# Kernel optimization log

Measured on AMD Instinct MI355X. Metric: run time of the kernel, lower is better.

Reference implementation:

```python
import jax, jax.numpy as jnp
import numpy as np

B_, L_, D_ = 2, 4096, 1024
E_ = 2
DI = E_ * D_            # 2048
H_ = 16
HD_ = DI // H_          # 128
N_ = 128
K_ = 4                  # d_conv
CS_ = 256               # SSD chunk size
MC_ = 256               # Hebbian memory chunk size
ALPHA = 0.5             # memory_alpha (== write_alpha default)


def _silu(x):
    return x * jax.nn.sigmoid(x)


def _rmsnorm(x, w, eps=1e-6):
    return x * jax.lax.rsqrt(jnp.mean(x * x, axis=-1, keepdims=True) + eps) * w


def setup_inputs() -> dict:
    key = jax.random.key(0)
    ks = jax.random.split(key, 8)
    proj_dim = 2 * DI + 2 * H_ * N_ + H_
    n = lambda k, sh, sc: jax.random.normal(k, sh, jnp.float32) * sc
    return {
        "x": n(ks[0], (B_, L_, D_), 1.0),
        "norm_w": jnp.ones((D_,), jnp.float32),
        "w_in": n(ks[1], (proj_dim, D_), 0.02),
        "conv_w": n(ks[2], (DI, K_), 0.2),
        "conv_b": jnp.zeros((DI,), jnp.float32),
        "A_log": jnp.log(2.0 * jnp.ones((H_,), jnp.float32)),
        "dt_bias": jnp.zeros((H_,), jnp.float32),
        "D_skip": jnp.ones((DI,), jnp.float32),
        "w_out": n(ks[3], (D_, DI), 0.02),
        "w_write": n(ks[4], (D_, D_), 0.02),
        "w_read": n(ks[5], (D_, D_), 0.02),
        "decay": jnp.float32(4.6),
    }


def _forward(x, norm_w, w_in, conv_w, conv_b, A_log, dt_bias, D_skip,
             w_out, w_write, w_read, decay):
    B, L, D = x.shape
    residual = x
    xn = _rmsnorm(x, norm_w)

    # ---- SSDBlock ----
    proj = xn @ w_in.T  # (B,L,2*DI+2*H*N+H)
    val = proj[..., :DI]
    gate = proj[..., DI:2 * DI]
    Bp = proj[..., 2 * DI:2 * DI + H_ * N_].reshape(B, L, H_, N_)
    Cp = proj[..., 2 * DI + H_ * N_:2 * DI + 2 * H_ * N_].reshape(B, L, H_, N_)
    dt = jax.nn.softplus(proj[..., -H_:] + dt_bias)  # (B,L,H)

    # causal depthwise conv1d (kernel K_, groups=DI)
    vp = jnp.pad(val, ((0, 0), (K_ - 1, 0), (0, 0)))
    val = sum(conv_w[:, k] * vp[:, k:k + L, :] for k in range(K_)) + conv_b
    val = _silu(val).reshape(B, L, H_, HD_)

    ld = dt * (-jnp.exp(A_log))  # log decay (B,L,H)

    nc = L // CS_
    to_chunks = lambda a: jnp.moveaxis(a.reshape(B, nc, CS_, *a.shape[2:]), 1, 0)
    tril = jnp.tril(jnp.ones((CS_, CS_), bool))
    Dv = D_skip.reshape(1, H_, 1, HD_)

    def ssd_chunk(h, inp):
        v_c, b_c, c_c, ld_c = inp  # (B,CS,H,HD), (B,CS,H,N), (B,CS,H,N), (B,CS,H)
        cum = jnp.cumsum(ld_c, axis=1)            # (B,CS,H)
        cum_h = jnp.transpose(cum, (0, 2, 1))     # (B,H,CS)
        dd = cum_h[:, :, :, None] - cum_h[:, :, None, :]
        Lmat = jnp.where(tril, jnp.exp(dd), 0.0)
        M = jnp.einsum('blhn,bmhn->bhlm', c_c, b_c) * Lmat
        v_h = jnp.transpose(v_c, (0, 2, 1, 3))    # (B,H,CS,HD)
        Y = M @ v_h
        Y = Y + jnp.einsum('blhn,bhdn,blh->bhld', c_c, h, jnp.exp(cum))
        Y = Y + Dv * v_h
        h = jnp.exp(cum[:, -1])[:, :, None, None] * h + \
            jnp.einsum('blhd,blhn,blh->bhdn', v_c, b_c, jnp.exp(cum[:, -1:, :] - cum))
        return h, Y

    h0 = jnp.zeros((B, H_, HD_, N_), jnp.float32)
    _, Ys = jax.lax.scan(ssd_chunk, h0,
                         (to_chunks(val), to_chunks(Bp), to_chunks(Cp), to_chunks(ld)))
    # (nc,B,H,CS,HD) -> (B,L,DI)
    Y = jnp.transpose(Ys, (1, 0, 3, 2, 4)).reshape(B, L, DI)
    out = (Y * _silu(gate)) @ w_out.T  # (B,L,D)

    # ---- Hebbian memory (chunkwise) ----
    gamma = jax.nn.sigmoid(decay)
    lg = jnp.log(gamma)
    v = out @ w_write.T
    wk = jnp.pad(out[:, :-1], ((0, 0), (1, 0), (0, 0)))  # shifted write keys
    p = jnp.arange(MC_)
    diffs = jnp.maximum(p[:, None] - 1 - p[None, :], 0).astype(jnp.float32)
    causal = (p[:, None] > p[None, :]).astype(jnp.float32)
    Mmem = jnp.exp(diffs * lg) * causal
    gp = gamma ** p                    # read decay by position in chunk
    gw = gamma ** (MC_ - 1 - p)        # write decay to end of chunk
    nm = L // MC_
    tom = lambda a: jnp.moveaxis(a.reshape(B, nm, MC_, D), 1, 0)

    def mem_chunk(W, inp):
        rk_c, wk_c, v_c = inp  # (B,MC,D)
        inter = jnp.einsum('bde,bte->btd', W, rk_c) * gp[None, :, None]
        S = jnp.einsum('bie,bje->bij', rk_c, wk_c)
        intra = (S * Mmem) @ v_c
        W = gamma ** MC_ * W + jnp.einsum('btd,bte->bde', v_c * gw[None, :, None], wk_c)
        return W, inter + intra

    W0 = jnp.zeros((B, D, D), jnp.float32)
    _, reads = jax.lax.scan(mem_chunk, W0, (tom(out), tom(wk), tom(v)))
    reads = jnp.moveaxis(reads, 0, 1).reshape(B, L, D)
    out = out + ALPHA * (reads @ w_read.T)
    return residual + out


def reference(x, norm_w, w_in, conv_w, conv_b, A_log, dt_bias, D_skip,
              w_out, w_write, w_read, decay):
    return _forward(x, norm_w, w_in, conv_w, conv_b, A_log, dt_bias, D_skip,
                    w_out, w_write, w_read, decay)
```

## Files before the change

kernel.cpp:

```cpp
#include <hip/hip_runtime.h>
#include <hip/hip_bf16.h>

typedef __hip_bfloat16 bf16;
typedef __attribute__((ext_vector_type(8))) short short8;
typedef __attribute__((ext_vector_type(4))) float floatx4;
typedef __attribute__((ext_vector_type(16))) float floatx16;

#define B_ 2
#define L_ 4096
#define D_ 1024
#define DI_ 2048
#define H_ 16
#define HD_ 128
#define N_ 128
#define CS_ 256
#define MC_ 256
#define NC_ 16
#define PROJ_ 8208

__device__ __forceinline__ float bf2f(short s) {
    return __uint_as_float(((unsigned)(unsigned short)s) << 16);
}

__device__ __forceinline__ void gl_lds16(const void* g, void* s) {
    __builtin_amdgcn_global_load_lds(
        (const __attribute__((address_space(1))) void*)g,
        (__attribute__((address_space(3))) void*)s, 16, 0, 0);
}

struct GemmP {
    const bf16* A; const bf16* Bt;
    float* C; bf16* CB; bf16* CB2; bf16* CB3;
    const float* add0; const float* add1; const bf16* add0b; const float* scr;
    long lda, ldb, ldc;
    int M, N, K, zinner;
    long a_zo, a_zi, b_zo, b_zi, c_zo, c_zi;
};

template<int EPI>
__global__ __launch_bounds__(256, 2) void gemm_bt(GemmP p)
{
    int NT = gridDim.x, MT = gridDim.y;
    long T = (long)NT * MT * gridDim.z;
    long flat = ((long)blockIdx.z * MT + blockIdx.y) * NT + blockIdx.x;
    int xcd = (int)(flat & 7);
    long q = flat >> 3;
    long Tq = T >> 3; int Tr = (int)(T & 7);
    long tile = (long)xcd * Tq + (long)(xcd < Tr ? xcd : Tr) + q;
    long per_z = (long)NT * MT;
    int z = (int)(tile / per_z);
    int t2 = (int)(tile - (long)z * per_z);
    int FG = NT >> 3;
    int g, width, within;
    if (t2 < FG * MT * 8) { g = t2 / (MT * 8); width = 8; within = t2 - g * MT * 8; }
    else                  { g = FG; width = NT - FG * 8; within = t2 - FG * MT * 8; }
    int m_outer = within / (8 * width);
    int hb = MT - m_outer * 8; if (hb > 8) hb = 8;
    int inner = within - m_outer * 8 * width;
    int n_in = inner / hb, m_in = inner - n_in * hb;
    int m0 = (m_outer * 8 + m_in) * 128;
    int n0 = (g * 8 + n_in) * 128;

    int zo = z / p.zinner, zi = z % p.zinner;
    const bf16* A  = p.A  + (long)zo * p.a_zo + (long)zi * p.a_zi;
    const bf16* Bt = p.Bt + (long)zo * p.b_zo + (long)zi * p.b_zi;
    long coff = (long)zo * p.c_zo + (long)zi * p.c_zi;

    __shared__ __align__(16) bf16 As[128 * 64];
    __shared__ __align__(16) bf16 Bs[128 * 64];

    int tid = threadIdx.x;
    int lane = tid & 63, wave = tid >> 6;
    int wm = (wave >> 1) * 64, wn = (wave & 1) * 64;
    int ln31 = lane & 31, hi = lane >> 5;

    floatx16 acc[2][2];
#pragma unroll
    for (int i = 0; i < 2; i++)
#pragma unroll
        for (int j = 0; j < 2; j++)
#pragma unroll
            for (int r = 0; r < 16; r++) acc[i][j][r] = 0.f;

    int lrow = lane >> 3;
    int lc = ((lane & 7) ^ lrow) * 8;
    int wrow = wave * 32;
    int rx = lane & 7;

    for (int k0 = 0; k0 < p.K; k0 += 64) {
#pragma unroll
        for (int t = 0; t < 4; t++) {
            int row = wrow + t * 8 + lrow;
            gl_lds16(A + (long)(m0 + row) * p.lda + k0 + lc, &As[(wrow + t * 8) * 64]);
            int bn = n0 + row; if (bn > p.N - 1) bn = p.N - 1;
            gl_lds16(Bt + (long)bn * p.ldb + k0 + lc, &Bs[(wrow + t * 8) * 64]);
        }
        __syncthreads();
#pragma unroll
        for (int ks = 0; ks < 64; ks += 16) {
            int lb = (ks >> 3) + hi;
            int po = ((lb ^ rx) << 3);
            short8 af[2], bq[2];
#pragma unroll
            for (int i = 0; i < 2; i++)
                af[i] = *(const short8*)&As[(wm + i * 32 + ln31) * 64 + po];
#pragma unroll
            for (int j = 0; j < 2; j++)
                bq[j] = *(const short8*)&Bs[(wn + j * 32 + ln31) * 64 + po];
#pragma unroll
            for (int i = 0; i < 2; i++)
#pragma unroll
                for (int j = 0; j < 2; j++)
                    acc[i][j] = __builtin_amdgcn_mfma_f32_32x32x16_bf16(af[i], bq[j], acc[i][j], 0, 0, 0);
        }
        __syncthreads();
    }

#pragma unroll
    for (int i = 0; i < 2; i++) {
#pragma unroll
        for (int j = 0; j < 2; j++) {
#pragma unroll
            for (int r = 0; r < 16; r++) {
                int gm = m0 + wm + i * 32 + (r & 3) + 8 * (r >> 2) + 4 * hi;
                int gn = n0 + wn + j * 32 + ln31;
                if (gm >= p.M || gn >= p.N) continue;
                float a = acc[i][j][r];
                if (EPI == 0) {
                    p.C[coff + (long)gm * p.ldc + gn] = a;
                } else if (EPI == 2) {
                    if (gn < 2048)      p.CB [(long)gm * 2048 + gn]          = __float2bfloat16(a);
                    else if (gn < 4096) p.CB2[(long)gm * 2048 + (gn - 2048)] = __float2bfloat16(a);
                    else if (gn < 8192) p.CB3[(long)gm * 4096 + (gn - 4096)] = __float2bfloat16(a);
                    else                p.C  [(long)gm * 16   + (gn - 8192)] = a;
                } else if (EPI == 3) {
                    float lg = p.scr[1];
                    float v = (gm > gn) ? a * __expf((float)(gm - 1 - gn) * lg) : 0.f;
                    p.CB[coff + (long)gm * p.ldc + gn] = __float2bfloat16(v);
                } else if (EPI == 4) {
                    long ix = coff + (long)gm * p.ldc + gn;
                    float t = a * p.scr[16 + gm] + __bfloat162float(p.add0b[ix]);
                    p.CB[ix] = __float2bfloat16(t);
                } else if (EPI == 6) {
                    p.CB[coff + (long)gm * p.ldc + gn] = __float2bfloat16(a);
                } else if (EPI == 7) {
                    long ix = (long)gm * p.ldc + gn;
                    p.C[ix] = p.add0[ix] + __bfloat162float(p.add0b[ix]) + 0.5f * a;
                } else if (EPI == 8) {
                    long ix = (long)gm * p.ldc + gn;
                    bf16 v = __float2bfloat16(a);
                    p.CB[ix] = v;
                    int l = gm & (L_ - 1);
                    if (l != L_ - 1) p.CB2[ix + p.ldc] = v;
                    if (l == 0) p.CB2[ix] = __float2bfloat16(0.f);
                }
            }
        }
    }
}

__global__ void k_gamma(const float* decay, float* scr)
{
    int t = threadIdx.x;
    float g = 1.f / (1.f + expf(-decay[0]));
    float lg = logf(g);
    if (t == 0) { scr[0] = g; scr[1] = lg; scr[2] = expf(256.f * lg); }
    scr[16 + t]  = expf(lg * (float)t);
    scr[272 + t] = expf(lg * (float)(255 - t));
}

__global__ void k_f2ball(const float* __restrict__ s0, bf16* __restrict__ d0, long n0,
                         const float* __restrict__ s1, bf16* __restrict__ d1, long n1,
                         const float* __restrict__ s2, bf16* __restrict__ d2, long n2,
                         const float* __restrict__ s3, bf16* __restrict__ d3, long n3)
{
    long i = (long)blockIdx.x * 256 + threadIdx.x;
    const float* s; bf16* d; long rel = i;
    if (rel < n0) { s = s0; d = d0; }
    else { rel -= n0;
        if (rel < n1) { s = s1; d = d1; }
        else { rel -= n1;
            if (rel < n2) { s = s2; d = d2; }
            else { rel -= n2; if (rel >= n3) return; s = s3; d = d3; }
        }
    }
    float4 v = ((const float4*)s)[rel];
    bf16* o = d + rel * 4;
    o[0] = __float2bfloat16(v.x); o[1] = __float2bfloat16(v.y);
    o[2] = __float2bfloat16(v.z); o[3] = __float2bfloat16(v.w);
}

__global__ __launch_bounds__(256) void k_rmsnorm(const float* __restrict__ x,
                                                 const float* __restrict__ w,
                                                 bf16* __restrict__ o)
{
    int row = blockIdx.x, t = threadIdx.x;
    float4 xv = ((const float4*)(x + (long)row * D_))[t];
    float s = xv.x*xv.x + xv.y*xv.y + xv.z*xv.z + xv.w*xv.w;
#pragma unroll
    for (int m = 32; m > 0; m >>= 1) s += __shfl_xor(s, m, 64);
    __shared__ float ps[4];
    if ((t & 63) == 0) ps[t >> 6] = s;
    __syncthreads();
    s = ps[0] + ps[1] + ps[2] + ps[3];
    float r = rsqrtf(s * (1.f / (float)D_) + 1e-6f);
    float4 wv = ((const float4*)w)[t];
    bf16* orow = o + (long)row * D_ + t * 4;
    orow[0] = __float2bfloat16(xv.x * r * wv.x);
    orow[1] = __float2bfloat16(xv.y * r * wv.y);
    orow[2] = __float2bfloat16(xv.z * r * wv.z);
    orow[3] = __float2bfloat16(xv.w * r * wv.w);
}

__global__ __launch_bounds__(256) void k_cum(const float* __restrict__ dtr,
                                             const float* __restrict__ dt_bias,
                                             const float* __restrict__ A_log,
                                             float* __restrict__ cum_g,
                                             float* __restrict__ cumlast)
{
    int bid = blockIdx.x;
    int h = bid & 15, c = (bid >> 4) & 15, b = bid >> 8;
    long rowbase = (long)b * L_ + c * CS_;
    int tid = threadIdx.x;
    __shared__ float cum_s[256];
    float d = dtr[(rowbase + tid) * H_ + h] + dt_bias[h];
    float sp = (d > 20.f) ? d : log1pf(__expf(d));
    cum_s[tid] = -__expf(A_log[h]) * sp;
    __syncthreads();
    for (int off = 1; off < 256; off <<= 1) {
        float add = (tid >= off) ? cum_s[tid - off] : 0.f;
        __syncthreads();
        cum_s[tid] += add;
        __syncthreads();
    }
    cum_g[(rowbase + tid) * H_ + h] = cum_s[tid];
    if (tid == 255) cumlast[bid] = cum_s[255];
}

__global__ void k_vtc(const bf16* __restrict__ val_b, const float* __restrict__ cw,
                      const float* __restrict__ cb, bf16* __restrict__ vT)
{
    __shared__ bf16 tile[35][33];
    int b = blockIdx.z;
    int r0 = blockIdx.x * 32, c0 = blockIdx.y * 32;
    int tid = threadIdx.x;
    for (int idx = tid; idx < 35 * 32; idx += 256) {
        int row = idx >> 5, ch = idx & 31;
        int gl = r0 - 3 + row;
        bf16 v = __float2bfloat16(0.f);
        if (gl >= 0 && gl < L_) v = val_b[((long)b * L_ + gl) * 2048 + c0 + ch];
        tile[row][ch] = v;
    }
    __syncthreads();
    int tx = tid & 31, ty = tid >> 5;
    int l = r0 + tx;
    for (int i = 0; i < 32; i += 8) {
        int ch = c0 + ty + i;
        float4 cwv = ((const float4*)cw)[ch];
        float acc = cb[ch]
                  + cwv.x * __bfloat162float(tile[tx][ty + i])
                  + cwv.y * __bfloat162float(tile[tx + 1][ty + i])
                  + cwv.z * __bfloat162float(tile[tx + 2][ty + i])
                  + cwv.w * __bfloat162float(tile[tx + 3][ty + i]);
        float s = acc / (1.f + __expf(-acc));
        vT[((long)b * 2048 + ch) * L_ + l] = __float2bfloat16(s);
    }
}

__global__ void k_bt(const bf16* __restrict__ bc, bf16* __restrict__ BT)
{
    __shared__ bf16 tile[32][33];
    int b = blockIdx.z;
    int r0 = blockIdx.x * 32, c0 = blockIdx.y * 32;
    int tx = threadIdx.x & 31, ty = threadIdx.x >> 5;
    for (int i = 0; i < 32; i += 8)
        tile[ty + i][tx] = bc[((long)b * L_ + r0 + ty + i) * 4096 + c0 + tx];
    __syncthreads();
    int l = r0 + tx;
    for (int i = 0; i < 32; i += 8) {
        int col = c0 + ty + i;
        BT[((long)b * 2048 + col) * L_ + l] = tile[tx][ty + i];
    }
}

__global__ __launch_bounds__(256, 2) void k_ssd_u2(
    const bf16* __restrict__ vT, const bf16* __restrict__ BT,
    const float* __restrict__ cum_g, const float* __restrict__ cumlast,
    float* __restrict__ U)
{
    int bid = blockIdx.x;
    int h = bid & 15, c = (bid >> 4) & 15, b = bid >> 8;
    long rowbase = (long)b * L_ + c * CS_;
    int tid = threadIdx.x;
    __shared__ float w_s[256];
    w_s[tid] = __expf(cumlast[bid] - cum_g[(rowbase + tid) * H_ + h]);
    __syncthreads();
    int lane = tid & 63, wave = tid >> 6;
    int r16 = lane & 15, q8 = (lane >> 4) * 8, rq = (lane >> 4) * 4;
    int d0 = (wave >> 1) * 64, n0 = (wave & 1) * 64;
    const bf16* vb = vT + ((long)b * 2048 + h * 128) * L_ + c * 256;
    const bf16* bb = BT + ((long)b * 2048 + h * 128) * L_ + c * 256;
    floatx4 zero4 = {0.f, 0.f, 0.f, 0.f};
    floatx4 acc[4][4];
#pragma unroll
    for (int i = 0; i < 4; i++)
#pragma unroll
        for (int j = 0; j < 4; j++) acc[i][j] = zero4;
#pragma unroll 2
    for (int ks = 0; ks < 8; ks++) {
        float wv[8];
#pragma unroll
        for (int j = 0; j < 8; j++) wv[j] = w_s[ks * 32 + q8 + j];
        short8 af[4], bq[4];
#pragma unroll
        for (int i = 0; i < 4; i++) {
            short8 raw = *(const short8*)(vb + (long)(d0 + i * 16 + r16) * L_ + ks * 32 + q8);
#pragma unroll
            for (int j = 0; j < 8; j++) {
                float f = bf2f(raw[j]) * wv[j];
                raw[j] = (short)(__float_as_uint(f) >> 16);
            }
            af[i] = raw;
        }
#pragma unroll
        for (int j = 0; j < 4; j++)
            bq[j] = *(const short8*)(bb + (long)(n0 + j * 16 + r16) * L_ + ks * 32 + q8);
#pragma unroll
        for (int i = 0; i < 4; i++)
#pragma unroll
            for (int j = 0; j < 4; j++)
                acc[i][j] = __builtin_amdgcn_mfma_f32_16x16x32_bf16(af[i], bq[j], acc[i][j], 0, 0, 0);
    }
    float* up = U + (((long)c * B_ + b) * H_ + h) * 16384;
#pragma unroll
    for (int i = 0; i < 4; i++)
#pragma unroll
        for (int j = 0; j < 4; j++)
#pragma unroll
            for (int r = 0; r < 4; r++)
                up[(d0 + i * 16 + rq + r) * 128 + (n0 + j * 16 + r16)] = acc[i][j][r];
}

__global__ void k_ssd2(const float* __restrict__ U, const float* __restrict__ cumlast,
                       bf16* __restrict__ hst)
{
    long idx = (long)blockIdx.x * 256 + threadIdx.x;
    const long tot = (long)B_ * H_ * HD_ * N_;
    if (idx >= tot) return;
    int bh = (int)(idx >> 14);
    int b = bh >> 4, h = bh & 15;
    float hv = 0.f;
    for (int c = 0; c < NC_; c++) {
        hst[c * tot + idx] = __float2bfloat16(hv);
        float ef = __expf(cumlast[b * 256 + c * 16 + h]);
        hv = ef * hv + U[c * tot + idx];
    }
}

__global__ __launch_bounds__(256, 2) void k_ssd_y(
    const bf16* __restrict__ bc_b, const bf16* __restrict__ vT,
    const bf16* __restrict__ hst, const float* __restrict__ cum_g,
    const float* __restrict__ Dskip, const bf16* __restrict__ gate_b,
    bf16* __restrict__ yg)
{
    int bid = blockIdx.x;
    int h = bid & 15, c = (bid >> 4) & 15, b = bid >> 8;
    long rowbase = (long)b * L_ + c * CS_;
    int tid = threadIdx.x, lane = tid & 63, wave = tid >> 6;
    int r16 = lane & 15, q8 = (lane >> 4) * 8, rq = (lane >> 4) * 4;
    int wt = (wave >> 1) * 32, wmS = (wave & 1) * 32, wd = (wave & 1) * 64;

    __shared__ float cum_s[256];
    __shared__ __align__(16) bf16 Ss[64][72];

    cum_s[tid] = cum_g[(rowbase + tid) * H_ + h];
    __syncthreads();

    const bf16* Cb  = bc_b + rowbase * 4096 + 2048 + h * 128;
    const bf16* Bb  = bc_b + rowbase * 4096 + h * 128;
    const bf16* vTb = vT + ((long)b * 2048 + h * 128) * L_ + c * 256;
    const bf16* hp  = hst + (((long)c * B_ + b) * H_ + h) * 16384;

    floatx4 zero4 = {0.f, 0.f, 0.f, 0.f};

    for (int tt = 0; tt < 4; tt++) {
        int tbase = tt * 64;
        short8 caf[2][4];
#pragma unroll
        for (int i = 0; i < 2; i++)
#pragma unroll
            for (int ks = 0; ks < 4; ks++)
                caf[i][ks] = *(const short8*)(Cb + (long)(tbase + wt + i * 16 + r16) * 4096 + ks * 32 + q8);

        floatx4 yacc[2][4];
#pragma unroll
        for (int i = 0; i < 2; i++)
#pragma unroll
            for (int j = 0; j < 4; j++) yacc[i][j] = zero4;
#pragma unroll
        for (int ks = 0; ks < 4; ks++)
#pragma unroll
            for (int j = 0; j < 4; j++) {
                short8 hq = *(const short8*)(hp + (long)(wd + j * 16 + r16) * 128 + ks * 32 + q8);
#pragma unroll
                for (int i = 0; i < 2; i++)
                    yacc[i][j] = __builtin_amdgcn_mfma_f32_16x16x32_bf16(caf[i][ks], hq, yacc[i][j], 0, 0, 0);
            }
        float texp[2][4];
#pragma unroll
        for (int i = 0; i < 2; i++)
#pragma unroll
            for (int r = 0; r < 4; r++)
                texp[i][r] = __expf(cum_s[tbase + wt + i * 16 + rq + r]);
#pragma unroll
        for (int i = 0; i < 2; i++)
#pragma unroll
            for (int j = 0; j < 4; j++)
#pragma unroll
                for (int r = 0; r < 4; r++) yacc[i][j][r] *= texp[i][r];

        for (int mt = 0; mt <= tt; mt++) {
            int mbase = mt * 64;
            floatx4 sacc[2][2];
#pragma unroll
            for (int i = 0; i < 2; i++)
#pragma unroll
                for (int j = 0; j < 2; j++) sacc[i][j] = zero4;
#pragma unroll
            for (int ks = 0; ks < 4; ks++) {
                short8 bq[2];
#pragma unroll
                for (int j = 0; j < 2; j++)
                    bq[j] = *(const short8*)(Bb + (long)(mbase + wmS + j * 16 + r16) * 4096 + ks * 32 + q8);
#pragma unroll
                for (int i = 0; i < 2; i++)
#pragma unroll
                    for (int j = 0; j < 2; j++)
                        sacc[i][j] = __builtin_amdgcn_mfma_f32_16x16x32_bf16(caf[i][ks], bq[j], sacc[i][j], 0, 0, 0);
            }
            __syncthreads();
#pragma unroll
            for (int i = 0; i < 2; i++)
#pragma unroll
                for (int r = 0; r < 4; r++) {
                    int trow = wt + i * 16 + rq + r;
                    float ct = cum_s[tbase + trow];
#pragma unroll
                    for (int j = 0; j < 2; j++) {
                        int mcol = mbase + wmS + j * 16 + r16;
                        float val = (mcol <= tbase + trow) ? sacc[i][j][r] * __expf(ct - cum_s[mcol]) : 0.f;
                        Ss[trow][wmS + j * 16 + r16] = __float2bfloat16(val);
                    }
                }
            __syncthreads();
#pragma unroll
            for (int ks = 0; ks < 2; ks++) {
                short8 saf[2];
#pragma unroll
                for (int i = 0; i < 2; i++)
                    saf[i] = *(const short8*)&Ss[wt + i * 16 + r16][ks * 32 + q8];
#pragma unroll
                for (int j = 0; j < 4; j++) {
                    short8 vq = *(const short8*)(vTb + (long)(wd + j * 16 + r16) * L_ + mbase + ks * 32 + q8);
#pragma unroll
                    for (int i = 0; i < 2; i++)
                        yacc[i][j] = __builtin_amdgcn_mfma_f32_16x16x32_bf16(saf[i], vq, yacc[i][j], 0, 0, 0);
                }
            }
        }
#pragma unroll
        for (int i = 0; i < 2; i++)
#pragma unroll
            for (int r = 0; r < 4; r++) {
                int t = tbase + wt + i * 16 + rq + r;
                long grow = (rowbase + t) * 2048 + h * 128;
#pragma unroll
                for (int j = 0; j < 4; j++) {
                    int d = wd + j * 16 + r16;
                    float vv = __bfloat162float(vTb[(long)d * L_ + t]);
                    float y = yacc[i][j][r] + Dskip[h * 128 + d] * vv;
                    float g = __bfloat162float(gate_b[grow + d]);
                    float sg = g / (1.f + __expf(-g));
                    yg[grow + d] = __float2bfloat16(y * sg);
                }
            }
    }
}

__global__ void k_transpose_b(const bf16* __restrict__ srcg, bf16* __restrict__ dstg)
{
    __shared__ bf16 t[32][33];
    int b = blockIdx.z;
    const bf16* src = srcg + (long)b * L_ * D_;
    bf16* dst = dstg + (long)b * D_ * L_;
    int r0 = blockIdx.x * 32, c0 = blockIdx.y * 32;
    int tx = threadIdx.x & 31, ty = threadIdx.x >> 5;
    for (int i = 0; i < 32; i += 8)
        t[ty + i][tx] = src[(long)(r0 + ty + i) * D_ + c0 + tx];
    __syncthreads();
    for (int i = 0; i < 32; i += 8)
        dst[(long)(c0 + ty + i) * L_ + r0 + tx] = t[tx][ty + i];
}

__global__ void k_trans_wkg(const bf16* __restrict__ outg, const float* __restrict__ scr,
                            bf16* __restrict__ dstg)
{
    __shared__ float t[32][33];
    int b = blockIdx.z;
    const bf16* src = outg + (long)b * L_ * D_;
    bf16* dst = dstg + (long)b * D_ * L_;
    int r0 = blockIdx.x * 32, c0 = blockIdx.y * 32;
    int tx = threadIdx.x & 31, ty = threadIdx.x >> 5;
    for (int i = 0; i < 32; i += 8) {
        int rr = r0 + ty + i;
        float g = scr[272 + (rr & 255)];
        t[ty + i][tx] = (rr == 0) ? 0.f : __bfloat162float(src[(long)(rr - 1) * D_ + c0 + tx]) * g;
    }
    __syncthreads();
    for (int i = 0; i < 32; i += 8)
        dst[(long)(c0 + ty + i) * L_ + r0 + tx] = __float2bfloat16(t[tx][ty + i]);
}

__global__ void k_m2(bf16* __restrict__ UwW, const float* __restrict__ scr)
{
    long idx = (long)blockIdx.x * 256 + threadIdx.x;
    const long tot = (long)B_ * D_ * D_;
    if (idx >= tot) return;
    float gMC = scr[2];
    float w = 0.f;
    for (int c = 0; c < NC_; c++) {
        float tmp = __bfloat162float(UwW[c * tot + idx]);
        UwW[c * tot + idx] = __float2bfloat16(w);
        w = gMC * w + tmp;
    }
}

static inline int cdiv_i(long a, long b) { return (int)((a + b - 1) / b); }

static void run_gemm(hipStream_t st, int epi, const bf16* A, const bf16* Bt,
                     float* C, bf16* CB, bf16* CB2, bf16* CB3,
                     const float* add0, const float* add1, const bf16* add0b,
                     const float* scr, int M, int N, int K,
                     long lda, long ldb, long ldc, int nbatch, int zinner,
                     long a_zo, long a_zi, long b_zo, long b_zi, long c_zo, long c_zi)
{
    GemmP p;
    p.A = A; p.Bt = Bt; p.C = C; p.CB = CB; p.CB2 = CB2; p.CB3 = CB3;
    p.add0 = add0; p.add1 = add1; p.add0b = add0b; p.scr = scr;
    p.lda = lda; p.ldb = ldb; p.ldc = ldc;
    p.M = M; p.N = N; p.K = K; p.zinner = zinner;
    p.a_zo = a_zo; p.a_zi = a_zi; p.b_zo = b_zo; p.b_zi = b_zi; p.c_zo = c_zo; p.c_zi = c_zi;
    dim3 g(cdiv_i(N, 128), cdiv_i(M, 128), nbatch);
    dim3 b(256);
    switch (epi) {
        case 0: gemm_bt<0><<<g, b, 0, st>>>(p); break;
        case 2: gemm_bt<2><<<g, b, 0, st>>>(p); break;
        case 3: gemm_bt<3><<<g, b, 0, st>>>(p); break;
        case 4: gemm_bt<4><<<g, b, 0, st>>>(p); break;
        case 6: gemm_bt<6><<<g, b, 0, st>>>(p); break;
        case 7: gemm_bt<7><<<g, b, 0, st>>>(p); break;
        case 8: gemm_bt<8><<<g, b, 0, st>>>(p); break;
    }
}

extern "C" void kernel_launch(void* const* d_in, const int* in_sizes, int n_in,
                              void* d_out, int out_size, void* d_ws, size_t ws_size,
                              hipStream_t stream)
{
    const float* x       = (const float*)d_in[0];
    const float* norm_w  = (const float*)d_in[1];
    const float* w_in    = (const float*)d_in[2];
    const float* conv_w  = (const float*)d_in[3];
    const float* conv_b  = (const float*)d_in[4];
    const float* A_log   = (const float*)d_in[5];
    const float* dt_bias = (const float*)d_in[6];
    const float* D_skip  = (const float*)d_in[7];
    const float* w_out   = (const float*)d_in[8];
    const float* w_write = (const float*)d_in[9];
    const float* w_read  = (const float*)d_in[10];
    const float* decay   = (const float*)d_in[11];
    float* outp = (float*)d_out;

    const size_t SZ_SCR  = 4096;
    const size_t SZ_DT   = (size_t)B_ * L_ * H_ * 4;
    const size_t SZ_CUML = 2048;
    const size_t SZ_WOUT = (size_t)D_ * DI_ * 2;
    const size_t SZ_WSML = (size_t)D_ * D_ * 2;
    const size_t SZ_R1   = (size_t)B_ * L_ * 2048 * 2;
    const size_t SZ_R2   = SZ_R1;
    const size_t SZ_R3   = (size_t)B_ * L_ * 4096 * 2;
    const size_t SZ_R4   = (size_t)B_ * L_ * D_ * 2 + (size_t)PROJ_ * D_ * 2;
    const size_t SZ_R5   = (size_t)B_ * L_ * 2048 * 4;

    size_t o = 0;
    auto take = [&](size_t sz) { size_t r = o; o += (sz + 255) & ~(size_t)255; return r; };
    const size_t O_SCR = take(SZ_SCR);
    const size_t O_DT  = take(SZ_DT);
    const size_t O_LD  = take(SZ_DT);
    const size_t O_CUM = take(SZ_DT);
    const size_t O_CL  = take(SZ_CUML);
    const size_t O_WO  = take(SZ_WOUT);
    const size_t O_WW  = take(SZ_WSML);
    const size_t O_WR  = take(SZ_WSML);
    const size_t O_R1  = take(SZ_R1);
    const size_t O_R2  = take(SZ_R2);
    const size_t O_R3  = take(SZ_R3);
    const size_t O_R4  = take(SZ_R4);
    const size_t O_R5  = take(SZ_R5);
    const size_t NEED = o;
    if (ws_size < NEED) return;
    (void)O_LD;

    char* ws = (char*)d_ws;
    float* scr     = (float*)(ws + O_SCR);
    float* dt_raw  = (float*)(ws + O_DT);
    float* cum_g   = (float*)(ws + O_CUM);
    float* cumlast = (float*)(ws + O_CL);
    bf16*  w_out_b   = (bf16*)(ws + O_WO);
    bf16*  w_write_b = (bf16*)(ws + O_WW);
    bf16*  w_read_b  = (bf16*)(ws + O_WR);

    bf16*  val_b   = (bf16*)(ws + O_R1);
    bf16*  yg_b    = (bf16*)(ws + O_R1);
    bf16*  hst_b   = (bf16*)(ws + O_R1 + (size_t)B_ * L_ * D_ * 2);
    bf16*  Sm_b    = (bf16*)(ws + O_R1);
    bf16*  intra_b = (bf16*)(ws + O_R1 + (size_t)NC_ * B_ * MC_ * MC_ * 2);
    bf16*  gate_b  = (bf16*)(ws + O_R2);
    bf16*  out_b   = (bf16*)(ws + O_R2);
    bf16*  wk_b    = (bf16*)(ws + O_R2 + (size_t)B_ * L_ * D_ * 2);
    bf16*  reads_b = wk_b;
    bf16*  bc_b    = (bf16*)(ws + O_R3);
    bf16*  UwW     = (bf16*)(ws + O_R3);
    bf16*  xn_b    = (bf16*)(ws + O_R4);
    bf16*  w_in_b  = (bf16*)(ws + O_R4 + (size_t)B_ * L_ * D_ * 2);
    float* U_ssd   = (float*)(ws + O_R4);
    bf16*  vT_g    = (bf16*)(ws + O_R5);
    bf16*  BT_g    = (bf16*)(ws + O_R5 + (size_t)B_ * L_ * 2048 * 2);
    bf16*  vbuf_b  = (bf16*)(ws + O_R5);
    bf16*  vTm     = (bf16*)(ws + O_R5 + (size_t)B_ * L_ * D_ * 4);
    bf16*  wkgT    = (bf16*)(ws + O_R5 + (size_t)B_ * L_ * D_ * 4 + (size_t)B_ * L_ * D_ * 2);

    k_gamma<<<1, 256, 0, stream>>>(decay, scr);
    {
        long n0 = (long)PROJ_ * D_ / 4, n1 = (long)D_ * DI_ / 4;
        long n2 = (long)D_ * D_ / 4,   n3 = n2;
        k_f2ball<<<cdiv_i(n0 + n1 + n2 + n3, 256), 256, 0, stream>>>(
            w_in, w_in_b, n0, w_out, w_out_b, n1, w_write, w_write_b, n2, w_read, w_read_b, n3);
    }
    k_rmsnorm<<<B_ * L_, 256, 0, stream>>>(x, norm_w, xn_b);
    run_gemm(stream, 2, xn_b, w_in_b, dt_raw, val_b, gate_b, bc_b, nullptr, nullptr, nullptr, nullptr,
             B_ * L_, PROJ_, D_, D_, D_, 0, 1, 1, 0, 0, 0, 0, 0, 0);
    k_cum<<<B_ * NC_ * H_, 256, 0, stream>>>(dt_raw, dt_bias, A_log, cum_g, cumlast);
    k_vtc<<<dim3(L_ / 32, DI_ / 32, B_), 256, 0, stream>>>(val_b, conv_w, conv_b, vT_g);
    k_bt<<<dim3(L_ / 32, DI_ / 32, B_), 256, 0, stream>>>(bc_b, BT_g);
    k_ssd_u2<<<B_ * NC_ * H_, 256, 0, stream>>>(vT_g, BT_g, cum_g, cumlast, U_ssd);
    k_ssd2<<<cdiv_i((long)B_ * H_ * HD_ * N_, 256), 256, 0, stream>>>(U_ssd, cumlast, hst_b);
    k_ssd_y<<<B_ * NC_ * H_, 256, 0, stream>>>(bc_b, vT_g, hst_b, cum_g, D_skip, gate_b, yg_b);
    run_gemm(stream, 8, yg_b, w_out_b, nullptr, out_b, wk_b, nullptr, nullptr, nullptr, nullptr, nullptr,
             B_ * L_, D_, DI_, DI_, DI_, D_, 1, 1, 0, 0, 0, 0, 0, 0);
    run_gemm(stream, 6, out_b, w_write_b, nullptr, vbuf_b, nullptr, nullptr, nullptr, nullptr, nullptr, nullptr,
             B_ * L_, D_, D_, D_, D_, D_, 1, 1, 0, 0, 0, 0, 0, 0);
    k_transpose_b<<<dim3(L_ / 32, D_ / 32, B_), 256, 0, stream>>>(vbuf_b, vTm);
    k_trans_wkg<<<dim3(L_ / 32, D_ / 32, B_), 256, 0, stream>>>(out_b, scr, wkgT);
    run_gemm(stream, 6, vTm, wkgT, nullptr, UwW, nullptr, nullptr, nullptr, nullptr, nullptr, nullptr,
             D_, D_, MC_, L_, L_, D_, B_ * NC_, NC_,
             (long)D_ * L_, MC_, (long)D_ * L_, MC_, (long)D_ * D_, (long)B_ * D_ * D_);
    k_m2<<<cdiv_i((long)B_ * D_ * D_, 256), 256, 0, stream>>>(UwW, scr);
    run_gemm(stream, 3, out_b, wk_b, nullptr, Sm_b, nullptr, nullptr, nullptr, nullptr, nullptr, scr,
             MC_, MC_, D_, D_, D_, MC_, B_ * NC_, NC_,
             (long)L_ * D_, (long)MC_ * D_, (long)L_ * D_, (long)MC_ * D_,
             (long)MC_ * MC_, (long)B_ * MC_ * MC_);
    run_gemm(stream, 6, Sm_b, vTm, nullptr, intra_b, nullptr, nullptr, nullptr, nullptr, nullptr, nullptr,
             MC_, D_, MC_, MC_, L_, D_, B_ * NC_, NC_,
             (long)MC_ * MC_, (long)B_ * MC_ * MC_, (long)D_ * L_, MC_,
             (long)L_ * D_, (long)MC_ * D_);
    run_gemm(stream, 4, out_b, UwW, nullptr, reads_b, nullptr, nullptr, nullptr, nullptr, intra_b, scr,
             MC_, D_, D_, D_, D_, D_, B_ * NC_, NC_,
             (long)L_ * D_, (long)MC_ * D_, (long)D_ * D_, (long)B_ * D_ * D_,
             (long)L_ * D_, (long)MC_ * D_);
    run_gemm(stream, 7, reads_b, w_read_b, outp, nullptr, nullptr, nullptr, x, nullptr, out_b, nullptr,
             B_ * L_, D_, D_, D_, D_, D_, 1, 1, 0, 0, 0, 0, 0, 0);
}
```

Baseline: 748.5 us.

## Skip masked triangular GEMM tiles, store SSD states in bf16, vectorize scans, fuse transposes

Adds a triangular mode to the batched GEMM. Tiles of the causal score matrix that lie strictly above the diagonal are zero-filled without computing, and the following product stops its K loop at the diagonal. The SSD chunk-state buffer U now holds bf16 instead of fp32, and both chunk-recurrence scans handle 8 elements per thread with vector loads. The two memory transposes become one kernel. Together these cut masked-out MFMA work, memory traffic and launch count, at the cost of bf16 rounding on the intermediate SSD states.

```diff
diff --git a/kernel.cpp b/kernel.cpp
--- a/kernel.cpp
+++ b/kernel.cpp
@@ -21,6 +21,10 @@
 __device__ __forceinline__ float bf2f(short s) {
     return __uint_as_float(((unsigned)(unsigned short)s) << 16);
 }
+__device__ __forceinline__ short f2bf(float f) {
+    __hip_bfloat16 h = __float2bfloat16(f);
+    return *(short*)&h;
+}
 
 __device__ __forceinline__ void gl_lds16(const void* g, void* s) {
     __builtin_amdgcn_global_load_lds(
@@ -33,7 +37,7 @@
     float* C; bf16* CB; bf16* CB2; bf16* CB3;
     const float* add0; const float* add1; const bf16* add0b; const float* scr;
     long lda, ldb, ldc;
-    int M, N, K, zinner;
+    int M, N, K, zinner, tri;
     long a_zo, a_zi, b_zo, b_zi, c_zo, c_zi;
 };
 
@@ -66,14 +70,32 @@
     const bf16* Bt = p.Bt + (long)zo * p.b_zo + (long)zi * p.b_zi;
     long coff = (long)zo * p.c_zo + (long)zi * p.c_zi;
 
-    __shared__ __align__(16) bf16 As[128 * 64];
-    __shared__ __align__(16) bf16 Bs[128 * 64];
-
     int tid = threadIdx.x;
     int lane = tid & 63, wave = tid >> 6;
     int wm = (wave >> 1) * 64, wn = (wave & 1) * 64;
     int ln31 = lane & 31, hi = lane >> 5;
 
+    if (p.tri == 1 && n0 >= m0 + 128) {
+        if (EPI == 3) {
+#pragma unroll
+            for (int i = 0; i < 2; i++)
+#pragma unroll
+                for (int j = 0; j < 2; j++)
+#pragma unroll
+                    for (int r = 0; r < 16; r++) {
+                        int gm = m0 + wm + i * 32 + (r & 3) + 8 * (r >> 2) + 4 * hi;
+                        int gn = n0 + wn + j * 32 + ln31;
+                        if (gm < p.M && gn < p.N)
+                            p.CB[coff + (long)gm * p.ldc + gn] = __float2bfloat16(0.f);
+                    }
+        }
+        return;
+    }
+    int Keff = (p.tri == 2) ? (m0 + 128 < p.K ? m0 + 128 : p.K) : p.K;
+
+    __shared__ __align__(16) bf16 As[128 * 64];
+    __shared__ __align__(16) bf16 Bs[128 * 64];
+
     floatx16 acc[2][2];
 #pragma unroll
     for (int i = 0; i < 2; i++)
@@ -87,7 +109,7 @@
     int wrow = wave * 32;
     int rx = lane & 7;
 
-    for (int k0 = 0; k0 < p.K; k0 += 64) {
+    for (int k0 = 0; k0 < Keff; k0 += 64) {
 #pragma unroll
         for (int t = 0; t < 4; t++) {
             int row = wrow + t * 8 + lrow;
@@ -286,7 +308,7 @@
 __global__ __launch_bounds__(256, 2) void k_ssd_u2(
     const bf16* __restrict__ vT, const bf16* __restrict__ BT,
     const float* __restrict__ cum_g, const float* __restrict__ cumlast,
-    float* __restrict__ U)
+    bf16* __restrict__ U)
 {
     int bid = blockIdx.x;
     int h = bid & 15, c = (bid >> 4) & 15, b = bid >> 8;
@@ -331,29 +353,37 @@
             for (int j = 0; j < 4; j++)
                 acc[i][j] = __builtin_amdgcn_mfma_f32_16x16x32_bf16(af[i], bq[j], acc[i][j], 0, 0, 0);
     }
-    float* up = U + (((long)c * B_ + b) * H_ + h) * 16384;
+    bf16* up = U + (((long)c * B_ + b) * H_ + h) * 16384;
 #pragma unroll
     for (int i = 0; i < 4; i++)
 #pragma unroll
         for (int j = 0; j < 4; j++)
 #pragma unroll
             for (int r = 0; r < 4; r++)
-                up[(d0 + i * 16 + rq + r) * 128 + (n0 + j * 16 + r16)] = acc[i][j][r];
-}
-
-__global__ void k_ssd2(const float* __restrict__ U, const float* __restrict__ cumlast,
+                up[(d0 + i * 16 + rq + r) * 128 + (n0 + j * 16 + r16)] = __float2bfloat16(acc[i][j][r]);
+}
+
+__global__ void k_ssd2(const bf16* __restrict__ U, const float* __restrict__ cumlast,
                        bf16* __restrict__ hst)
 {
-    long idx = (long)blockIdx.x * 256 + threadIdx.x;
     const long tot = (long)B_ * H_ * HD_ * N_;
+    long idx = ((long)blockIdx.x * 256 + threadIdx.x) * 8;
     if (idx >= tot) return;
     int bh = (int)(idx >> 14);
     int b = bh >> 4, h = bh & 15;
-    float hv = 0.f;
+    float hv[8];
+#pragma unroll
+    for (int j = 0; j < 8; j++) hv[j] = 0.f;
     for (int c = 0; c < NC_; c++) {
-        hst[c * tot + idx] = __float2bfloat16(hv);
         float ef = __expf(cumlast[b * 256 + c * 16 + h]);
-        hv = ef * hv + U[c * tot + idx];
+        short8 u = *(const short8*)(U + c * tot + idx);
+        short8 o;
+#pragma unroll
+        for (int j = 0; j < 8; j++) {
+            o[j] = f2bf(hv[j]);
+            hv[j] = ef * hv[j] + bf2f(u[j]);
+        }
+        *(short8*)(hst + c * tot + idx) = o;
     }
 }
 
@@ -487,51 +517,52 @@
     }
 }
 
-__global__ void k_transpose_b(const bf16* __restrict__ srcg, bf16* __restrict__ dstg)
-{
-    __shared__ bf16 t[32][33];
+__global__ void k_trans2(const bf16* __restrict__ vbuf, const bf16* __restrict__ outg,
+                         const float* __restrict__ scr,
+                         bf16* __restrict__ vTm, bf16* __restrict__ wkgT)
+{
+    __shared__ bf16 tv[32][33];
+    __shared__ bf16 tw[32][33];
     int b = blockIdx.z;
-    const bf16* src = srcg + (long)b * L_ * D_;
-    bf16* dst = dstg + (long)b * D_ * L_;
-    int r0 = blockIdx.x * 32, c0 = blockIdx.y * 32;
-    int tx = threadIdx.x & 31, ty = threadIdx.x >> 5;
-    for (int i = 0; i < 32; i += 8)
-        t[ty + i][tx] = src[(long)(r0 + ty + i) * D_ + c0 + tx];
-    __syncthreads();
-    for (int i = 0; i < 32; i += 8)
-        dst[(long)(c0 + ty + i) * L_ + r0 + tx] = t[tx][ty + i];
-}
-
-__global__ void k_trans_wkg(const bf16* __restrict__ outg, const float* __restrict__ scr,
-                            bf16* __restrict__ dstg)
-{
-    __shared__ float t[32][33];
-    int b = blockIdx.z;
-    const bf16* src = outg + (long)b * L_ * D_;
-    bf16* dst = dstg + (long)b * D_ * L_;
+    const bf16* srcv = vbuf + (long)b * L_ * D_;
+    const bf16* srco = outg + (long)b * L_ * D_;
     int r0 = blockIdx.x * 32, c0 = blockIdx.y * 32;
     int tx = threadIdx.x & 31, ty = threadIdx.x >> 5;
     for (int i = 0; i < 32; i += 8) {
         int rr = r0 + ty + i;
+        tv[ty + i][tx] = srcv[(long)rr * D_ + c0 + tx];
         float g = scr[272 + (rr & 255)];
-        t[ty + i][tx] = (rr == 0) ? 0.f : __bfloat162float(src[(long)(rr - 1) * D_ + c0 + tx]) * g;
+        float w = (rr == 0) ? 0.f : __bfloat162float(srco[(long)(rr - 1) * D_ + c0 + tx]) * g;
+        tw[ty + i][tx] = __float2bfloat16(w);
     }
     __syncthreads();
-    for (int i = 0; i < 32; i += 8)
-        dst[(long)(c0 + ty + i) * L_ + r0 + tx] = __float2bfloat16(t[tx][ty + i]);
+    bf16* dv = vTm + (long)b * D_ * L_;
+    bf16* dw = wkgT + (long)b * D_ * L_;
+    for (int i = 0; i < 32; i += 8) {
+        long o = (long)(c0 + ty + i) * L_ + r0 + tx;
+        dv[o] = tv[tx][ty + i];
+        dw[o] = tw[tx][ty + i];
+    }
 }
 
 __global__ void k_m2(bf16* __restrict__ UwW, const float* __restrict__ scr)
 {
-    long idx = (long)blockIdx.x * 256 + threadIdx.x;
     const long tot = (long)B_ * D_ * D_;
+    long idx = ((long)blockIdx.x * 256 + threadIdx.x) * 8;
     if (idx >= tot) return;
     float gMC = scr[2];
-    float w = 0.f;
+    float w[8];
+#pragma unroll
+    for (int j = 0; j < 8; j++) w[j] = 0.f;
     for (int c = 0; c < NC_; c++) {
-        float tmp = __bfloat162float(UwW[c * tot + idx]);
-        UwW[c * tot + idx] = __float2bfloat16(w);
-        w = gMC * w + tmp;
+        short8 u = *(const short8*)(UwW + c * tot + idx);
+        short8 o;
+#pragma unroll
+        for (int j = 0; j < 8; j++) {
+            o[j] = f2bf(w[j]);
+            w[j] = gMC * w[j] + bf2f(u[j]);
+        }
+        *(short8*)(UwW + c * tot + idx) = o;
     }
 }
 
@@ -542,13 +573,14 @@
                      const float* add0, const float* add1, const bf16* add0b,
                      const float* scr, int M, int N, int K,
                      long lda, long ldb, long ldc, int nbatch, int zinner,
-                     long a_zo, long a_zi, long b_zo, long b_zi, long c_zo, long c_zi)
+                     long a_zo, long a_zi, long b_zo, long b_zi, long c_zo, long c_zi,
+                     int tri = 0)
 {
     GemmP p;
     p.A = A; p.Bt = Bt; p.C = C; p.CB = CB; p.CB2 = CB2; p.CB3 = CB3;
     p.add0 = add0; p.add1 = add1; p.add0b = add0b; p.scr = scr;
     p.lda = lda; p.ldb = ldb; p.ldc = ldc;
-    p.M = M; p.N = N; p.K = K; p.zinner = zinner;
+    p.M = M; p.N = N; p.K = K; p.zinner = zinner; p.tri = tri;
     p.a_zo = a_zo; p.a_zi = a_zi; p.b_zo = b_zo; p.b_zi = b_zi; p.c_zo = c_zo; p.c_zi = c_zi;
     dim3 g(cdiv_i(N, 128), cdiv_i(M, 128), nbatch);
     dim3 b(256);
@@ -633,7 +665,7 @@
     bf16*  UwW     = (bf16*)(ws + O_R3);
     bf16*  xn_b    = (bf16*)(ws + O_R4);
     bf16*  w_in_b  = (bf16*)(ws + O_R4 + (size_t)B_ * L_ * D_ * 2);
-    float* U_ssd   = (float*)(ws + O_R4);
+    bf16*  U_ssd   = (bf16*)(ws + O_R4);
     bf16*  vT_g    = (bf16*)(ws + O_R5);
     bf16*  BT_g    = (bf16*)(ws + O_R5 + (size_t)B_ * L_ * 2048 * 2);
     bf16*  vbuf_b  = (bf16*)(ws + O_R5);
@@ -654,26 +686,25 @@
     k_vtc<<<dim3(L_ / 32, DI_ / 32, B_), 256, 0, stream>>>(val_b, conv_w, conv_b, vT_g);
     k_bt<<<dim3(L_ / 32, DI_ / 32, B_), 256, 0, stream>>>(bc_b, BT_g);
     k_ssd_u2<<<B_ * NC_ * H_, 256, 0, stream>>>(vT_g, BT_g, cum_g, cumlast, U_ssd);
-    k_ssd2<<<cdiv_i((long)B_ * H_ * HD_ * N_, 256), 256, 0, stream>>>(U_ssd, cumlast, hst_b);
+    k_ssd2<<<cdiv_i((long)B_ * H_ * HD_ * N_ / 8, 256), 256, 0, stream>>>(U_ssd, cumlast, hst_b);
     k_ssd_y<<<B_ * NC_ * H_, 256, 0, stream>>>(bc_b, vT_g, hst_b, cum_g, D_skip, gate_b, yg_b);
     run_gemm(stream, 8, yg_b, w_out_b, nullptr, out_b, wk_b, nullptr, nullptr, nullptr, nullptr, nullptr,
              B_ * L_, D_, DI_, DI_, DI_, D_, 1, 1, 0, 0, 0, 0, 0, 0);
     run_gemm(stream, 6, out_b, w_write_b, nullptr, vbuf_b, nullptr, nullptr, nullptr, nullptr, nullptr, nullptr,
              B_ * L_, D_, D_, D_, D_, D_, 1, 1, 0, 0, 0, 0, 0, 0);
-    k_transpose_b<<<dim3(L_ / 32, D_ / 32, B_), 256, 0, stream>>>(vbuf_b, vTm);
-    k_trans_wkg<<<dim3(L_ / 32, D_ / 32, B_), 256, 0, stream>>>(out_b, scr, wkgT);
+    k_trans2<<<dim3(L_ / 32, D_ / 32, B_), 256, 0, stream>>>(vbuf_b, out_b, scr, vTm, wkgT);
     run_gemm(stream, 6, vTm, wkgT, nullptr, UwW, nullptr, nullptr, nullptr, nullptr, nullptr, nullptr,
              D_, D_, MC_, L_, L_, D_, B_ * NC_, NC_,
              (long)D_ * L_, MC_, (long)D_ * L_, MC_, (long)D_ * D_, (long)B_ * D_ * D_);
-    k_m2<<<cdiv_i((long)B_ * D_ * D_, 256), 256, 0, stream>>>(UwW, scr);
+    k_m2<<<cdiv_i((long)B_ * D_ * D_ / 8, 256), 256, 0, stream>>>(UwW, scr);
     run_gemm(stream, 3, out_b, wk_b, nullptr, Sm_b, nullptr, nullptr, nullptr, nullptr, nullptr, scr,
              MC_, MC_, D_, D_, D_, MC_, B_ * NC_, NC_,
              (long)L_ * D_, (long)MC_ * D_, (long)L_ * D_, (long)MC_ * D_,
-             (long)MC_ * MC_, (long)B_ * MC_ * MC_);
+             (long)MC_ * MC_, (long)B_ * MC_ * MC_, 1);
     run_gemm(stream, 6, Sm_b, vTm, nullptr, intra_b, nullptr, nullptr, nullptr, nullptr, nullptr, nullptr,
              MC_, D_, MC_, MC_, L_, D_, B_ * NC_, NC_,
              (long)MC_ * MC_, (long)B_ * MC_ * MC_, (long)D_ * L_, MC_,
-             (long)L_ * D_, (long)MC_ * D_);
+             (long)L_ * D_, (long)MC_ * D_, 2);
     run_gemm(stream, 4, out_b, UwW, nullptr, reads_b, nullptr, nullptr, nullptr, nullptr, intra_b, scr,
              MC_, D_, D_, D_, D_, D_, B_ * NC_, NC_,
              (long)L_ * D_, (long)MC_ * D_, (long)D_ * D_, (long)B_ * D_ * D_,
```

Measured after the change: 756.2 us. About the same (+1.0%).
